# Performance work log

Hardware: AMD Instinct MI355X
Metric: run time of the kernel (lower is better)

Reference implementation:

```python
import jax, jax.numpy as jnp
import numpy as np

K = 512          # fixed candidate budget (replaces dynamic torch.where)
THRESH = 0.6
IOU = 0.5
STRIDE = 2.0
OFFSET = 6.0
WIN = 12.0
SCALE = 0.6      # pyramid scale this pass represents (12/min_face_size)


def _conv(x, w, b):
    y = jax.lax.conv_general_dilated(x, w, (1, 1), 'VALID',
                                     dimension_numbers=('NCHW', 'OIHW', 'NCHW'))
    return y + b[None, :, None, None]


def _prelu(x, a):
    return jnp.where(x >= 0, x, a[None, :, None, None] * x)


def _maxpool2(x):
    return jax.lax.reduce_window(x, -jnp.inf, jax.lax.max,
                                 (1, 1, 2, 2), (1, 1, 2, 2), 'VALID')


def _nms(boxes, valid, thr):
    # torchvision-style greedy NMS over score-sorted boxes; `valid` marks live boxes.
    x1, y1, x2, y2 = boxes[:, 0], boxes[:, 1], boxes[:, 2], boxes[:, 3]
    areas = (x2 - x1) * (y2 - y1)
    n = boxes.shape[0]
    idxs = jnp.arange(n)

    def body(i, keep):
        xi1 = jnp.maximum(x1[i], x1); yi1 = jnp.maximum(y1[i], y1)
        xi2 = jnp.minimum(x2[i], x2); yi2 = jnp.minimum(y2[i], y2)
        inter = jnp.clip(xi2 - xi1, 0.0) * jnp.clip(yi2 - yi1, 0.0)
        iou = inter / (areas[i] + areas - inter + 1e-9)
        sup = (iou > thr) & (idxs > i) & keep[i]
        return keep & (~sup)

    return jax.lax.fori_loop(0, n, body, valid)


def setup_inputs() -> dict:
    key = jax.random.key(0)
    ks = jax.random.split(key, 14)
    d = {}
    d['x'] = jax.random.normal(ks[0], (1, 3, 2048, 2048), dtype=jnp.float32)
    d['w1'] = jax.random.normal(ks[1], (10, 3, 3, 3), dtype=jnp.float32) * 0.1
    d['b1'] = jax.random.normal(ks[2], (10,), dtype=jnp.float32) * 0.01
    d['p1'] = jax.random.uniform(ks[3], (10,), dtype=jnp.float32) * 0.25
    d['w2'] = jax.random.normal(ks[4], (16, 10, 3, 3), dtype=jnp.float32) * 0.1
    d['b2'] = jax.random.normal(ks[5], (16,), dtype=jnp.float32) * 0.01
    d['p2'] = jax.random.uniform(ks[6], (16,), dtype=jnp.float32) * 0.25
    d['w3'] = jax.random.normal(ks[7], (32, 16, 3, 3), dtype=jnp.float32) * 0.1
    d['b3'] = jax.random.normal(ks[8], (32,), dtype=jnp.float32) * 0.01
    d['p3'] = jax.random.uniform(ks[9], (32,), dtype=jnp.float32) * 0.25
    d['wa'] = jax.random.normal(ks[10], (2, 32, 1, 1), dtype=jnp.float32) * 0.1
    d['ba'] = jax.random.normal(ks[11], (2,), dtype=jnp.float32) * 0.01
    d['wb'] = jax.random.normal(ks[12], (4, 32, 1, 1), dtype=jnp.float32) * 0.1
    d['bb'] = jax.random.normal(ks[13], (4,), dtype=jnp.float32) * 0.01
    return d


def reference(x, w1, b1, p1, w2, b2, p2, w3, b3, p3, wa, ba, wb, bb):
    H, W = x.shape[2], x.shape[3]
    h = _prelu(_conv(x, w1, b1), p1)
    h = _maxpool2(h)
    h = _prelu(_conv(h, w2, b2), p2)
    h = _prelu(_conv(h, w3, b3), p3)
    cls = _conv(h, wa, ba)              # [1,2,hf,wf]
    reg = _conv(h, wb, bb)              # [1,4,hf,wf]
    prob = jax.nn.softmax(cls, axis=1)[0, 1]   # Softmax2d over channels, face prob
    hf, wf = prob.shape
    scores = prob.reshape(-1)
    regf = jnp.transpose(reg[0], (1, 2, 0)).reshape(-1, 4)
    # threshold gather -> fixed-size top-K with invalid slots at score -1
    masked = jnp.where(scores >= THRESH, scores, -1.0)
    top_s, idx = jax.lax.top_k(masked, K)
    reg_k = regf[idx]
    yy = (idx // wf).astype(jnp.float32)
    xx = (idx % wf).astype(jnp.float32)
    off_x = ((W - OFFSET * 2) % STRIDE) / 2.0 + OFFSET
    off_y = ((H - OFFSET * 2) % STRIDE) / 2.0 + OFFSET
    cx = (xx * STRIDE + off_x) / SCALE
    cy = (yy * STRIDE + off_y) / SCALE
    ww = WIN / SCALE                    # square 12x12 window / scale
    x1 = cx - ww / 2 + reg_k[:, 0] * ww
    y1 = cy - ww / 2 + reg_k[:, 1] * ww
    x2 = cx + ww / 2 + reg_k[:, 2] * ww
    y2 = cy + ww / 2 + reg_k[:, 3] * ww
    boxes = jnp.stack([x1, y1, x2, y2], axis=1)   # [K,4]
    valid = top_s >= THRESH
    keep = _nms(boxes, valid, IOU)                # per-scale NMS
    keep = _nms(boxes, keep, IOU + 0.2)           # final cross-scale NMS
    out = jnp.concatenate([boxes, top_s[:, None]], axis=1)
    return out * keep[:, None].astype(out.dtype)  # [K,5] boxes+score, zeroed if dropped
```

## Files before the change

### kernel.cpp

```cpp
#include <hip/hip_runtime.h>

typedef unsigned long long u64;
typedef unsigned int u32;

#define W1H 1023
#define W2H 1021
#define W3H 1019
#define NPIX (W3H * W3H)
#define IDXMASK 0xFFFFFull
#define PSTR 1024

#define NBINS 2048
#define HLO 0.3055f
#define HW_ 0.025f
#define HINV 40.0f
#define HDELTA 0.10f

#define W1OFF 0
#define B1OFF 270
#define P1OFF 280
#define W2OFF 290
#define B2OFF 1730
#define P2OFF 1746
#define W3OFF 1762
#define B3OFF 6370
#define P3OFF 6402
#define WAOFF 6434
#define BAOFF 6498
#define WBOFF 6500
#define BBOFF 6628
#define WDTOT 6632

__global__ __launch_bounds__(256) void k_prep(
    const float* __restrict__ w1, const float* __restrict__ b1, const float* __restrict__ p1,
    const float* __restrict__ w2, const float* __restrict__ b2, const float* __restrict__ p2,
    const float* __restrict__ w3, const float* __restrict__ b3, const float* __restrict__ p3,
    const float* __restrict__ wa, const float* __restrict__ ba,
    const float* __restrict__ wb, const float* __restrict__ bb,
    double* __restrict__ wd, int* __restrict__ ctrl, u32* __restrict__ ghist)
{
    int t = threadIdx.x;
    if (t < 2) ctrl[t] = 0;
    for (int i = t; i < NBINS; i += 256) ghist[i] = 0u;
    for (int i = t; i < 270; i += 256)  wd[W1OFF + i] = (double)w1[i];
    if (t < 10) { wd[B1OFF + t] = (double)b1[t]; wd[P1OFF + t] = (double)p1[t]; }
    for (int i = t; i < 1440; i += 256) wd[W2OFF + i] = (double)w2[i];
    if (t < 16) { wd[B2OFF + t] = (double)b2[t]; wd[P2OFF + t] = (double)p2[t]; }
    for (int i = t; i < 4608; i += 256) wd[W3OFF + i] = (double)w3[i];
    if (t < 32) { wd[B3OFF + t] = (double)b3[t]; wd[P3OFF + t] = (double)p3[t]; }
    if (t < 64)  wd[WAOFF + t] = (double)wa[t];
    if (t < 2)   wd[BAOFF + t] = (double)ba[t];
    if (t < 128) wd[WBOFF + t] = (double)wb[t];
    if (t < 4)   wd[BBOFF + t] = (double)bb[t];
}

__global__ __launch_bounds__(256) void k_conv1f(
    const float* __restrict__ x, const float* __restrict__ w1,
    const float* __restrict__ b1, const float* __restrict__ p1,
    float* __restrict__ P)
{
    __shared__ float sw[270];
    __shared__ float sb[10], sp[10];
    int t = threadIdx.y * 64 + threadIdx.x;
    for (int i = t; i < 270; i += 256) sw[i] = w1[i];
    if (t < 10) { sb[t] = b1[t]; sp[t] = p1[t]; }
    __syncthreads();
    int px = blockIdx.x * 64 + threadIdx.x;
    int py = blockIdx.y * 4 + threadIdx.y;
    if (px >= W1H || py >= W1H) return;
    int ix = px * 2, iy = py * 2;
    float acc[10][4];
    #pragma unroll
    for (int ch = 0; ch < 10; ++ch) { acc[ch][0]=0.f; acc[ch][1]=0.f; acc[ch][2]=0.f; acc[ch][3]=0.f; }
    for (int c = 0; c < 3; ++c) {
        float in[4][4];
        #pragma unroll
        for (int u = 0; u < 4; ++u) {
            const float* row = x + ((size_t)c * 2048 + (iy + u)) * 2048 + ix;
            in[u][0]=row[0]; in[u][1]=row[1]; in[u][2]=row[2]; in[u][3]=row[3];
        }
        #pragma unroll
        for (int ch = 0; ch < 10; ++ch) {
            const float* wp = sw + (ch * 3 + c) * 9;
            #pragma unroll
            for (int u = 0; u < 3; ++u)
                #pragma unroll
                for (int v = 0; v < 3; ++v) {
                    float w = wp[u * 3 + v];
                    acc[ch][0] = fmaf(in[u][v],         w, acc[ch][0]);
                    acc[ch][1] = fmaf(in[u][v + 1],     w, acc[ch][1]);
                    acc[ch][2] = fmaf(in[u + 1][v],     w, acc[ch][2]);
                    acc[ch][3] = fmaf(in[u + 1][v + 1], w, acc[ch][3]);
                }
        }
    }
    #pragma unroll
    for (int ch = 0; ch < 10; ++ch) {
        float m = fmaxf(fmaxf(acc[ch][0], acc[ch][1]), fmaxf(acc[ch][2], acc[ch][3])) + sb[ch];
        float r = m >= 0.f ? m : sp[ch] * m;
        P[((size_t)ch * W1H + py) * PSTR + px] = r;
    }
}

__global__ __launch_bounds__(256) void k_conv2f(
    const float* __restrict__ P, const float* __restrict__ w2,
    const float* __restrict__ b2, const float* __restrict__ p2,
    float* __restrict__ H2)
{
    __shared__ __align__(16) float sw[10 * 16 * 12];
    __shared__ float sb[16], sp[16];
    int tx = threadIdx.x, ty = threadIdx.y;
    int t = ty * 64 + tx;
    for (int i = t; i < 1440; i += 256) {
        int o = i / 90, r = i % 90, c = r / 9, k = r % 9;
        sw[(c * 16 + o) * 12 + k] = w2[i];
    }
    if (t < 16) { sb[t] = b2[t]; sp[t] = p2[t]; }
    __syncthreads();
    int py = blockIdx.y;
    int px_base = blockIdx.x * 512 + tx * 8;
    float acc[4][8];
    #pragma unroll
    for (int j = 0; j < 4; ++j)
        #pragma unroll
        for (int p = 0; p < 8; ++p) acc[j][p] = 0.f;

    for (int c = 0; c < 10; ++c) {
        float f[3][12];
        #pragma unroll
        for (int u = 0; u < 3; ++u) {
            const float* row = P + ((size_t)c * W1H + (py + u)) * PSTR + px_base;
            float4 a = *(const float4*)(row);
            float4 b = *(const float4*)(row + 4);
            float4 d = *(const float4*)(row + 8);
            f[u][0]=a.x; f[u][1]=a.y; f[u][2]=a.z;  f[u][3]=a.w;
            f[u][4]=b.x; f[u][5]=b.y; f[u][6]=b.z;  f[u][7]=b.w;
            f[u][8]=d.x; f[u][9]=d.y; f[u][10]=d.z; f[u][11]=d.w;
        }
        #pragma unroll
        for (int j = 0; j < 4; ++j) {
            int o = ty * 4 + j;
            const float4* wv = (const float4*)(sw + (c * 16 + o) * 12);
            float4 wA = wv[0], wB = wv[1], wC = wv[2];
            float w[9] = {wA.x,wA.y,wA.z,wA.w,wB.x,wB.y,wB.z,wB.w,wC.x};
            #pragma unroll
            for (int u = 0; u < 3; ++u)
                #pragma unroll
                for (int v = 0; v < 3; ++v) {
                    float wt = w[u*3+v];
                    #pragma unroll
                    for (int p = 0; p < 8; ++p)
                        acc[j][p] = fmaf(f[u][p+v], wt, acc[j][p]);
                }
        }
    }
    #pragma unroll
    for (int j = 0; j < 4; ++j) {
        int o = ty * 4 + j;
        float bb_ = sb[o], pp_ = sp[o];
        #pragma unroll
        for (int p = 0; p < 8; ++p) {
            int px = px_base + p;
            if (px < W2H) {
                float v = acc[j][p] + bb_;
                v = v >= 0.f ? v : pp_ * v;
                H2[((size_t)o * W2H + py) * PSTR + px] = v;
            }
        }
    }
}

__global__ __launch_bounds__(512, 2) void k_conv3f(
    const float* __restrict__ H2, const float* __restrict__ w3,
    const float* __restrict__ b3, const float* __restrict__ p3,
    const float* __restrict__ wa, const float* __restrict__ ba,
    float* __restrict__ Lg, u32* __restrict__ ghist)
{
    __shared__ __align__(16) float sw[16 * 32 * 12];
    __shared__ float spart[8][512];
    __shared__ u32 hist[NBINS];
    __shared__ float sb[32], sp[32], swd[32];
    __shared__ float slgb;
    int tx = threadIdx.x, ty = threadIdx.y;
    int t = ty * 64 + tx;
    for (int i = t; i < 4608; i += 512) {
        int o = i / 144, rem = i % 144, c = rem / 9, k = rem % 9;
        sw[(c * 32 + o) * 12 + k] = w3[i];
    }
    if (t < 32) { sb[t] = b3[t]; sp[t] = p3[t]; swd[t] = wa[32 + t] - wa[t]; }
    if (t == 0) slgb = ba[1] - ba[0];
    for (int i = t; i < NBINS; i += 512) hist[i] = 0u;
    __syncthreads();

    int py = blockIdx.y;
    int px_base = blockIdx.x * 512 + tx * 8;
    float acc[4][8];
    #pragma unroll
    for (int j = 0; j < 4; ++j)
        #pragma unroll
        for (int p = 0; p < 8; ++p) acc[j][p] = 0.f;

    for (int c = 0; c < 16; ++c) {
        float f[3][12];
        #pragma unroll
        for (int u = 0; u < 3; ++u) {
            const float* row = H2 + ((size_t)c * W2H + (py + u)) * PSTR + px_base;
            float4 a = *(const float4*)(row);
            float4 b = *(const float4*)(row + 4);
            float4 d = *(const float4*)(row + 8);
            f[u][0]=a.x; f[u][1]=a.y; f[u][2]=a.z;  f[u][3]=a.w;
            f[u][4]=b.x; f[u][5]=b.y; f[u][6]=b.z;  f[u][7]=b.w;
            f[u][8]=d.x; f[u][9]=d.y; f[u][10]=d.z; f[u][11]=d.w;
        }
        #pragma unroll
        for (int j = 0; j < 4; ++j) {
            int o = ty * 4 + j;
            const float4* wv = (const float4*)(sw + (c * 32 + o) * 12);
            float4 wA = wv[0], wB = wv[1], wC = wv[2];
            float w[9] = {wA.x,wA.y,wA.z,wA.w,wB.x,wB.y,wB.z,wB.w,wC.x};
            #pragma unroll
            for (int u = 0; u < 3; ++u)
                #pragma unroll
                for (int v = 0; v < 3; ++v) {
                    float wt = w[u*3+v];
                    #pragma unroll
                    for (int p = 0; p < 8; ++p)
                        acc[j][p] = fmaf(f[u][p+v], wt, acc[j][p]);
                }
        }
    }

    float partv[8];
    #pragma unroll
    for (int p = 0; p < 8; ++p) partv[p] = 0.f;
    #pragma unroll
    for (int j = 0; j < 4; ++j) {
        int o = ty * 4 + j;
        float bb_ = sb[o], pp_ = sp[o], wdd = swd[o];
        #pragma unroll
        for (int p = 0; p < 8; ++p) {
            float v = acc[j][p] + bb_;
            v = v >= 0.f ? v : pp_ * v;
            partv[p] = fmaf(wdd, v, partv[p]);
        }
    }
    #pragma unroll
    for (int p = 0; p < 8; ++p) spart[ty][tx * 8 + p] = partv[p];
    __syncthreads();

    {
        float lg = slgb;
        #pragma unroll
        for (int g = 0; g < 8; ++g) lg += spart[g][t];
        int px = blockIdx.x * 512 + t;
        if (px < W3H) {
            Lg[(size_t)py * W3H + px] = lg;
            if (lg >= HLO) {
                int bin = (int)((lg - HLO) * HINV);
                if (bin > NBINS - 1) bin = NBINS - 1;
                atomicAdd(&hist[bin], 1u);
            }
        }
    }
    __syncthreads();
    for (int i = t; i < NBINS; i += 512) {
        u32 v = hist[i];
        if (v) atomicAdd(&ghist[i], v);
    }
}

__global__ __launch_bounds__(256) void k_scan(
    const u32* __restrict__ ghist, int* __restrict__ ctrl)
{
    __shared__ u32 h[NBINS];
    __shared__ u32 tsum[256];
    __shared__ int best;
    int t = threadIdx.x;
    for (int i = t; i < NBINS; i += 256) h[i] = ghist[i];
    if (t == 0) best = -1;
    __syncthreads();
    u32 s = 0;
    #pragma unroll
    for (int k = 0; k < 8; ++k) s += h[t * 8 + k];
    tsum[t] = s;
    __syncthreads();
    for (int off = 1; off < 256; off <<= 1) {
        u32 add = (t + off < 256) ? tsum[t + off] : 0u;
        __syncthreads();
        tsum[t] += add;
        __syncthreads();
    }
    u32 cum = (t < 255) ? tsum[t + 1] : 0u;
    int cand = -1;
    for (int k = 7; k >= 0; --k) {
        cum += h[t * 8 + k];
        if (cand < 0 && cum >= 512) cand = t * 8 + k;
    }
    if (cand >= 0) atomicMax(&best, cand);
    __syncthreads();
    if (t == 0) {
        float T = (best < 0) ? HLO : (HLO + (float)best * HW_ - HDELTA);
        ((float*)ctrl)[2] = T;
    }
}

__global__ __launch_bounds__(256) void k_select(
    const float* __restrict__ Lg, int* __restrict__ ctrl, u32* __restrict__ selidx)
{
    float T = ((const float*)ctrl)[2];
    int stride = gridDim.x * 256;
    for (int i = blockIdx.x * 256 + threadIdx.x; i < NPIX; i += stride) {
        if (Lg[i] >= T) {
            int slot = atomicAdd(&ctrl[0], 1);
            selidx[slot] = (u32)i;
        }
    }
}

__global__ __launch_bounds__(64) void k_recomp(
    const float* __restrict__ x, const double* __restrict__ wd,
    const u32* __restrict__ selidx, int* __restrict__ ctrl,
    u64* __restrict__ keys, double* __restrict__ boxplane)
{
    __shared__ double xw[3][12][12];
    __shared__ double Pw[10][5][5];
    __shared__ double Hw[16][3][3];
    __shared__ double vch[32];
    int nsel = ctrl[0]; if (nsel > NPIX) nsel = NPIX;
    int t = threadIdx.x;
    for (int s = blockIdx.x; s < nsel; s += gridDim.x) {
        u32 idx = selidx[s];
        int y3 = (int)(idx / W3H), x3 = (int)(idx % W3H);
        int xr = 2 * y3, xc = 2 * x3;
        for (int i = t; i < 432; i += 64) {
            int c = i / 144, r = (i % 144) / 12, cc = i % 12;
            xw[c][r][cc] = (double)x[((size_t)c * 2048 + (xr + r)) * 2048 + (xc + cc)];
        }
        __syncthreads();
        for (int i = t; i < 250; i += 64) {
            int ch = i / 25, py = (i % 25) / 5, px = i % 5;
            int r0 = py * 2, c0 = px * 2;
            double a00=0.0, a01=0.0, a10=0.0, a11=0.0;
            for (int c = 0; c < 3; ++c) {
                const double* wp = wd + W1OFF + (ch * 3 + c) * 9;
                #pragma unroll
                for (int u = 0; u < 3; ++u)
                    #pragma unroll
                    for (int v = 0; v < 3; ++v) {
                        double w = wp[u * 3 + v];
                        a00 = fma(xw[c][r0+u][c0+v],     w, a00);
                        a01 = fma(xw[c][r0+u][c0+v+1],   w, a01);
                        a10 = fma(xw[c][r0+u+1][c0+v],   w, a10);
                        a11 = fma(xw[c][r0+u+1][c0+v+1], w, a11);
                    }
            }
            double m = fmax(fmax(a00, a01), fmax(a10, a11)) + wd[B1OFF + ch];
            Pw[ch][py][px] = m >= 0.0 ? m : wd[P1OFF + ch] * m;
        }
        __syncthreads();
        for (int i = t; i < 144; i += 64) {
            int o = i / 9, hy = (i % 9) / 3, hx = i % 3;
            double acc = 0.0;
            for (int c = 0; c < 10; ++c) {
                const double* wp = wd + W2OFF + (o * 10 + c) * 9;
                #pragma unroll
                for (int k = 0; k < 9; ++k)
                    acc = fma(Pw[c][hy + k / 3][hx + k % 3], wp[k], acc);
            }
            acc += wd[B2OFF + o];
            Hw[o][hy][hx] = acc >= 0.0 ? acc : wd[P2OFF + o] * acc;
        }
        __syncthreads();
        if (t < 32) {
            double acc = 0.0;
            for (int c = 0; c < 16; ++c) {
                const double* wp = wd + W3OFF + (t * 16 + c) * 9;
                #pragma unroll
                for (int k = 0; k < 9; ++k)
                    acc = fma(Hw[c][k / 3][k % 3], wp[k], acc);
            }
            acc += wd[B3OFF + t];
            vch[t] = acc >= 0.0 ? acc : wd[P3OFF + t] * acc;
        }
        __syncthreads();
        if (t == 0) {
            double c0 = wd[BAOFF + 0], c1 = wd[BAOFF + 1];
            for (int o = 0; o < 32; ++o) {
                c0 = fma(wd[WAOFF + o], vch[o], c0);
                c1 = fma(wd[WAOFF + 32 + o], vch[o], c1);
            }
            double mx = fmax(c0, c1);
            double e0 = exp(c0 - mx), e1 = exp(c1 - mx);
            double prob = e1 / (e0 + e1);
            if (prob >= 0.6) {
                double r0 = wd[BBOFF+0], r1 = wd[BBOFF+1], r2 = wd[BBOFF+2], r3 = wd[BBOFF+3];
                for (int o = 0; o < 32; ++o) {
                    double v = vch[o];
                    r0 = fma(wd[WBOFF + o], v, r0);
                    r1 = fma(wd[WBOFF + 32 + o], v, r1);
                    r2 = fma(wd[WBOFF + 64 + o], v, r2);
                    r3 = fma(wd[WBOFF + 96 + o], v, r3);
                }
                double fx = (double)x3, fy = (double)y3;
                double cx = (fx * 2.0 + 6.0) / 0.6;
                double cy = (fy * 2.0 + 6.0) / 0.6;
                double ww = 12.0 / 0.6, hw = ww / 2.0;
                double* bp = boxplane + (size_t)idx * 5;
                bp[0] = cx - hw + r0 * ww;
                bp[1] = cy - hw + r1 * ww;
                bp[2] = cx + hw + r2 * ww;
                bp[3] = cy + hw + r3 * ww;
                bp[4] = prob;
                u64 bits = (u64)__double_as_longlong(prob);
                u64 kh = (bits - 0x3FE0000000000000ull) >> 9;
                int slot = atomicAdd(&ctrl[1], 1);
                keys[slot] = (kh << 20) | ((u64)(~idx) & IDXMASK);
            }
        }
        __syncthreads();
    }
}

__global__ __launch_bounds__(512) void k_sortchunks(
    const u64* __restrict__ cand, const int* __restrict__ ctrl,
    u64* __restrict__ sorted)
{
    __shared__ u64 stop_[512];
    __shared__ u64 schunk[512];
    int tid = threadIdx.x;
    int n = ctrl[1]; if (n > NPIX) n = NPIX;
    long base0 = (long)blockIdx.x * 2048;
    stop_[tid] = 0ull;
    if (base0 < n) {
        for (int s = 0; s < 4; ++s) {
            long base = base0 + (long)s * 512;
            if (base >= n) break;
            schunk[tid] = (base + tid < n) ? cand[base + tid] : 0ull;
            for (int k = 2; k <= 512; k <<= 1)
                for (int j = k >> 1; j > 0; j >>= 1) {
                    __syncthreads();
                    int ixj = tid ^ j;
                    if (ixj > tid) {
                        u64 a = schunk[tid], b = schunk[ixj];
                        bool desc = ((tid & k) == 0);
                        if (desc ? (a < b) : (a > b)) { schunk[tid] = b; schunk[ixj] = a; }
                    }
                }
            __syncthreads();
            u64 m = stop_[tid], v = schunk[511 - tid];
            stop_[tid] = m > v ? m : v;
            for (int j = 256; j > 0; j >>= 1) {
                __syncthreads();
                int ixj = tid ^ j;
                if (ixj > tid) {
                    u64 a = stop_[tid], b = stop_[ixj];
                    if (a < b) { stop_[tid] = b; stop_[ixj] = a; }
                }
            }
            __syncthreads();
        }
    }
    sorted[(size_t)blockIdx.x * 512 + tid] = stop_[tid];
}

__global__ __launch_bounds__(512) void k_merge8(
    const u64* __restrict__ in, u64* __restrict__ out, int nin)
{
    __shared__ u64 s[512];
    int tid = threadIdx.x;
    int base = blockIdx.x * 8;
    s[tid] = (base < nin) ? in[(size_t)base * 512 + tid] : 0ull;
    for (int c = 1; c < 8; ++c) {
        int li = base + c;
        u64 v = (li < nin) ? in[(size_t)li * 512 + (511 - tid)] : 0ull;
        __syncthreads();
        u64 m = s[tid];
        s[tid] = m > v ? m : v;
        for (int j = 256; j > 0; j >>= 1) {
            __syncthreads();
            int ixj = tid ^ j;
            if (ixj > tid) {
                u64 a = s[tid], b = s[ixj];
                if (a < b) { s[tid] = b; s[ixj] = a; }
            }
        }
        __syncthreads();
    }
    out[(size_t)blockIdx.x * 512 + tid] = s[tid];
}

__global__ __launch_bounds__(512) void k_boxmat(
    const u64* __restrict__ lists, const double* __restrict__ boxplane,
    u64* __restrict__ mats, double* __restrict__ bxs, u64* __restrict__ validw)
{
    __shared__ double sx1[512], sy1[512], sx2[512], sy2[512], sar[512];
    int tid = threadIdx.x;
    u64 key = lists[tid];
    bool valid = key != 0ull;
    double x1 = 0.0, y1 = 0.0, x2 = 0.0, y2 = 0.0, score = 0.0;
    if (valid) {
        u32 idx = (u32)(IDXMASK - (key & IDXMASK));
        const double* bp = boxplane + (size_t)idx * 5;
        x1 = bp[0]; y1 = bp[1]; x2 = bp[2]; y2 = bp[3]; score = bp[4];
    }
    double area = (x2 - x1) * (y2 - y1);
    sx1[tid] = x1; sy1[tid] = y1; sx2[tid] = x2; sy2[tid] = y2; sar[tid] = area;
    if (blockIdx.x == 0 && blockIdx.y == 0) {
        bxs[tid] = x1; bxs[512 + tid] = y1; bxs[1024 + tid] = x2;
        bxs[1536 + tid] = y2; bxs[2048 + tid] = score;
        u64 bal = __ballot(valid);
        if ((tid & 63) == 0) validw[tid >> 6] = bal;
    }
    __syncthreads();
    double thr = (blockIdx.y == 0) ? 0.5 : 0.7;
    int wv = tid >> 6;
    int rowbase = blockIdx.x * 64;
    for (int r = 0; r < 64; ++r) {
        int i = rowbase + r;
        double ix1 = fmax(sx1[i], x1);
        double iy1 = fmax(sy1[i], y1);
        double ix2 = fmin(sx2[i], x2);
        double iy2 = fmin(sy2[i], y2);
        double inter = fmax(ix2 - ix1, 0.0) * fmax(iy2 - iy1, 0.0);
        double uni = sar[i] + area - inter + 1e-9;
        bool sup = (uni > 0.0) && (inter > thr * uni) && (tid > i);
        u64 w = __ballot(sup);
        if ((tid & 63) == 0)
            mats[((size_t)blockIdx.y * 512 + i) * 8 + wv] = w;
    }
}

__global__ __launch_bounds__(512) void k_nmsfin(
    const u64* __restrict__ mats, const double* __restrict__ bxs,
    const u64* __restrict__ validw, float* __restrict__ out)
{
    __shared__ u64 keepw[8];
    int tid = threadIdx.x;
    if (tid < 8) keepw[tid] = validw[tid];
    __syncthreads();
    for (int pass = 0; pass < 2; ++pass) {
        if (tid < 64) {
            const u64* mat = mats + (size_t)pass * 512 * 8;
            u64 kw = (tid < 8) ? keepw[tid] : 0ull;
            for (int i = 0; i < 512; ++i) {
                u64 row = mat[i * 8 + (tid & 7)];
                u64 cur = __shfl(kw, i >> 6);
                if ((cur >> (i & 63)) & 1) kw &= ~row;
            }
            if (tid < 8) keepw[tid] = kw;
        }
        __syncthreads();
    }
    double kf = ((keepw[tid >> 6] >> (tid & 63)) & 1) ? 1.0 : 0.0;
    out[tid * 5 + 0] = (float)(bxs[tid] * kf);
    out[tid * 5 + 1] = (float)(bxs[512 + tid] * kf);
    out[tid * 5 + 2] = (float)(bxs[1024 + tid] * kf);
    out[tid * 5 + 3] = (float)(bxs[1536 + tid] * kf);
    out[tid * 5 + 4] = (float)(bxs[2048 + tid] * kf);
}

extern "C" void kernel_launch(void* const* d_in, const int* in_sizes, int n_in,
                              void* d_out, int out_size, void* d_ws, size_t ws_size,
                              hipStream_t stream)
{
    const float* x  = (const float*)d_in[0];
    const float* w1 = (const float*)d_in[1];
    const float* b1 = (const float*)d_in[2];
    const float* p1 = (const float*)d_in[3];
    const float* w2 = (const float*)d_in[4];
    const float* b2 = (const float*)d_in[5];
    const float* p2 = (const float*)d_in[6];
    const float* w3 = (const float*)d_in[7];
    const float* b3 = (const float*)d_in[8];
    const float* p3 = (const float*)d_in[9];
    const float* wa = (const float*)d_in[10];
    const float* ba = (const float*)d_in[11];
    const float* wb = (const float*)d_in[12];
    const float* bb = (const float*)d_in[13];
    float* out = (float*)d_out;

    char* ws = (char*)d_ws;
    float*  Pf    = (float*) (ws);
    float*  H2f   = (float*) (ws + 41902080);
    float*  Lg    = (float*) (ws + 108814336);
    u32*    ghist = (u32*)   (ws + 112967936);
    int*    ctrl  = (int*)   (ws + 112976128);
    u32*    selidx= (u32*)   (ws + 112976384);
    u64*    keys  = (u64*)   (ws + 117129984);
    u64*    sorted= (u64*)   (ws + 125437184);
    u64*    l1out = (u64*)   (ws + 127517952);
    u64*    l2out = (u64*)   (ws + 127780096);
    double* boxpl = (double*)(ws + 127812864);
    double* wd    = (double*)(ws + 169347584);
    u64*    l3out = (u64*)   (ws + 125437184);
    u64*    mats  = (u64*)   (ws + 125441280);
    double* bxs   = (double*)(ws + 125506816);
    u64*    vwords= (u64*)   (ws + 125527296);

    k_prep<<<1, 256, 0, stream>>>(w1, b1, p1, w2, b2, p2, w3, b3, p3, wa, ba, wb, bb, wd, ctrl, ghist);
    k_conv1f<<<dim3(16, 256), dim3(64, 4), 0, stream>>>(x, w1, b1, p1, Pf);
    k_conv2f<<<dim3(2, W2H), dim3(64, 4), 0, stream>>>(Pf, w2, b2, p2, H2f);
    k_conv3f<<<dim3(2, W3H), dim3(64, 8), 0, stream>>>(H2f, w3, b3, p3, wa, ba, Lg, ghist);
    k_scan<<<1, 256, 0, stream>>>(ghist, ctrl);
    k_select<<<1024, 256, 0, stream>>>(Lg, ctrl, selidx);
    k_recomp<<<2048, 64, 0, stream>>>(x, wd, selidx, ctrl, keys, boxpl);
    k_sortchunks<<<508, 512, 0, stream>>>(keys, ctrl, sorted);
    k_merge8<<<64, 512, 0, stream>>>(sorted, l1out, 508);
    k_merge8<<<8, 512, 0, stream>>>(l1out, l2out, 64);
    k_merge8<<<1, 512, 0, stream>>>(l2out, l3out, 8);
    k_boxmat<<<dim3(8, 2), 512, 0, stream>>>(l3out, boxpl, mats, bxs, vwords);
    k_nmsfin<<<1, 512, 0, stream>>>(mats, bxs, vwords, out);
}
```

Baseline: 601.0 us.

## Stage conv1 input in LDS, widen conv2/conv3 channel tiles, fuse scan into select

conv1 now loads its input tile into shared memory once, so neighbouring threads no longer issue overlapping scalar global loads. conv2 and conv3 give each thread 8 output channels instead of 4, and each block covers a full row with half as many blocks, so every loaded input row is reused across more channels. The histogram scan is folded into the select kernel, with every block redoing the scan, which removes one launch. The cost is higher register pressure from the 8x8 accumulators, which may lower occupancy, and fewer blocks for conv2 and conv3.

```diff
diff --git a/kernel.cpp b/kernel.cpp
--- a/kernel.cpp
+++ b/kernel.cpp
@@ -61,14 +61,25 @@
 {
     __shared__ float sw[270];
     __shared__ float sb[10], sp[10];
-    int t = threadIdx.y * 64 + threadIdx.x;
+    __shared__ float xs[3][10][132];
+    int tx = threadIdx.x, ty = threadIdx.y;
+    int t = ty * 64 + tx;
     for (int i = t; i < 270; i += 256) sw[i] = w1[i];
     if (t < 10) { sb[t] = b1[t]; sp[t] = p1[t]; }
-    __syncthreads();
-    int px = blockIdx.x * 64 + threadIdx.x;
-    int py = blockIdx.y * 4 + threadIdx.y;
+    int bx = blockIdx.x, by = blockIdx.y;
+    const float4* x4 = (const float4*)x;
+    for (int i = t; i < 990; i += 256) {
+        int c = i / 330, rem = i % 330, r = rem / 33, k = rem % 33;
+        int row = 8 * by + r; if (row > 2047) row = 2047;
+        int col4 = bx * 32 + k; if (col4 > 511) col4 = 511;
+        float4 v = x4[((size_t)c * 2048 + row) * 512 + col4];
+        xs[c][r][k * 4 + 0] = v.x; xs[c][r][k * 4 + 1] = v.y;
+        xs[c][r][k * 4 + 2] = v.z; xs[c][r][k * 4 + 3] = v.w;
+    }
+    __syncthreads();
+    int px = bx * 64 + tx;
+    int py = by * 4 + ty;
     if (px >= W1H || py >= W1H) return;
-    int ix = px * 2, iy = py * 2;
     float acc[10][4];
     #pragma unroll
     for (int ch = 0; ch < 10; ++ch) { acc[ch][0]=0.f; acc[ch][1]=0.f; acc[ch][2]=0.f; acc[ch][3]=0.f; }
@@ -76,8 +87,10 @@
         float in[4][4];
         #pragma unroll
         for (int u = 0; u < 4; ++u) {
-            const float* row = x + ((size_t)c * 2048 + (iy + u)) * 2048 + ix;
-            in[u][0]=row[0]; in[u][1]=row[1]; in[u][2]=row[2]; in[u][3]=row[3];
+            in[u][0] = xs[c][2*ty+u][2*tx+0];
+            in[u][1] = xs[c][2*ty+u][2*tx+1];
+            in[u][2] = xs[c][2*ty+u][2*tx+2];
+            in[u][3] = xs[c][2*ty+u][2*tx+3];
         }
         #pragma unroll
         for (int ch = 0; ch < 10; ++ch) {
@@ -118,10 +131,11 @@
     if (t < 16) { sb[t] = b2[t]; sp[t] = p2[t]; }
     __syncthreads();
     int py = blockIdx.y;
-    int px_base = blockIdx.x * 512 + tx * 8;
-    float acc[4][8];
-    #pragma unroll
-    for (int j = 0; j < 4; ++j)
+    int och0 = (ty & 1) * 8;
+    int px_base = (ty >> 1) * 512 + tx * 8;
+    float acc[8][8];
+    #pragma unroll
+    for (int j = 0; j < 8; ++j)
         #pragma unroll
         for (int p = 0; p < 8; ++p) acc[j][p] = 0.f;
 
@@ -138,8 +152,8 @@
             f[u][8]=d.x; f[u][9]=d.y; f[u][10]=d.z; f[u][11]=d.w;
         }
         #pragma unroll
-        for (int j = 0; j < 4; ++j) {
-            int o = ty * 4 + j;
+        for (int j = 0; j < 8; ++j) {
+            int o = och0 + j;
             const float4* wv = (const float4*)(sw + (c * 16 + o) * 12);
             float4 wA = wv[0], wB = wv[1], wC = wv[2];
             float w[9] = {wA.x,wA.y,wA.z,wA.w,wB.x,wB.y,wB.z,wB.w,wC.x};
@@ -155,8 +169,8 @@
         }
     }
     #pragma unroll
-    for (int j = 0; j < 4; ++j) {
-        int o = ty * 4 + j;
+    for (int j = 0; j < 8; ++j) {
+        int o = och0 + j;
         float bb_ = sb[o], pp_ = sp[o];
         #pragma unroll
         for (int p = 0; p < 8; ++p) {
@@ -177,7 +191,7 @@
     float* __restrict__ Lg, u32* __restrict__ ghist)
 {
     __shared__ __align__(16) float sw[16 * 32 * 12];
-    __shared__ float spart[8][512];
+    __shared__ float spart[4][1024];
     __shared__ u32 hist[NBINS];
     __shared__ float sb[32], sp[32], swd[32];
     __shared__ float slgb;
@@ -193,10 +207,11 @@
     __syncthreads();
 
     int py = blockIdx.y;
-    int px_base = blockIdx.x * 512 + tx * 8;
-    float acc[4][8];
-    #pragma unroll
-    for (int j = 0; j < 4; ++j)
+    int och0 = (ty & 3) * 8;
+    int px_base = (ty >> 2) * 512 + tx * 8;
+    float acc[8][8];
+    #pragma unroll
+    for (int j = 0; j < 8; ++j)
         #pragma unroll
         for (int p = 0; p < 8; ++p) acc[j][p] = 0.f;
 
@@ -213,8 +228,8 @@
             f[u][8]=d.x; f[u][9]=d.y; f[u][10]=d.z; f[u][11]=d.w;
         }
         #pragma unroll
-        for (int j = 0; j < 4; ++j) {
-            int o = ty * 4 + j;
+        for (int j = 0; j < 8; ++j) {
+            int o = och0 + j;
             const float4* wv = (const float4*)(sw + (c * 32 + o) * 12);
             float4 wA = wv[0], wB = wv[1], wC = wv[2];
             float w[9] = {wA.x,wA.y,wA.z,wA.w,wB.x,wB.y,wB.z,wB.w,wC.x};
@@ -234,8 +249,8 @@
     #pragma unroll
     for (int p = 0; p < 8; ++p) partv[p] = 0.f;
     #pragma unroll
-    for (int j = 0; j < 4; ++j) {
-        int o = ty * 4 + j;
+    for (int j = 0; j < 8; ++j) {
+        int o = och0 + j;
         float bb_ = sb[o], pp_ = sp[o], wdd = swd[o];
         #pragma unroll
         for (int p = 0; p < 8; ++p) {
@@ -245,16 +260,17 @@
         }
     }
     #pragma unroll
-    for (int p = 0; p < 8; ++p) spart[ty][tx * 8 + p] = partv[p];
-    __syncthreads();
-
-    {
+    for (int p = 0; p < 8; ++p) spart[ty & 3][px_base + p] = partv[p];
+    __syncthreads();
+
+    #pragma unroll
+    for (int rep = 0; rep < 2; ++rep) {
+        int pl = t + rep * 512;
         float lg = slgb;
         #pragma unroll
-        for (int g = 0; g < 8; ++g) lg += spart[g][t];
-        int px = blockIdx.x * 512 + t;
-        if (px < W3H) {
-            Lg[(size_t)py * W3H + px] = lg;
+        for (int g = 0; g < 4; ++g) lg += spart[g][pl];
+        if (pl < W3H) {
+            Lg[(size_t)py * W3H + pl] = lg;
             if (lg >= HLO) {
                 int bin = (int)((lg - HLO) * HINV);
                 if (bin > NBINS - 1) bin = NBINS - 1;
@@ -269,12 +285,14 @@
     }
 }
 
-__global__ __launch_bounds__(256) void k_scan(
-    const u32* __restrict__ ghist, int* __restrict__ ctrl)
+__global__ __launch_bounds__(256) void k_select(
+    const float* __restrict__ Lg, const u32* __restrict__ ghist,
+    int* __restrict__ ctrl, u32* __restrict__ selidx)
 {
     __shared__ u32 h[NBINS];
     __shared__ u32 tsum[256];
     __shared__ int best;
+    __shared__ float sT;
     int t = threadIdx.x;
     for (int i = t; i < NBINS; i += 256) h[i] = ghist[i];
     if (t == 0) best = -1;
@@ -298,18 +316,11 @@
     }
     if (cand >= 0) atomicMax(&best, cand);
     __syncthreads();
-    if (t == 0) {
-        float T = (best < 0) ? HLO : (HLO + (float)best * HW_ - HDELTA);
-        ((float*)ctrl)[2] = T;
-    }
-}
-
-__global__ __launch_bounds__(256) void k_select(
-    const float* __restrict__ Lg, int* __restrict__ ctrl, u32* __restrict__ selidx)
-{
-    float T = ((const float*)ctrl)[2];
+    if (t == 0) sT = (best < 0) ? HLO : (HLO + (float)best * HW_ - HDELTA);
+    __syncthreads();
+    float T = sT;
     int stride = gridDim.x * 256;
-    for (int i = blockIdx.x * 256 + threadIdx.x; i < NPIX; i += stride) {
+    for (int i = blockIdx.x * 256 + t; i < NPIX; i += stride) {
         if (Lg[i] >= T) {
             int slot = atomicAdd(&ctrl[0], 1);
             selidx[slot] = (u32)i;
@@ -599,10 +610,9 @@
 
     k_prep<<<1, 256, 0, stream>>>(w1, b1, p1, w2, b2, p2, w3, b3, p3, wa, ba, wb, bb, wd, ctrl, ghist);
     k_conv1f<<<dim3(16, 256), dim3(64, 4), 0, stream>>>(x, w1, b1, p1, Pf);
-    k_conv2f<<<dim3(2, W2H), dim3(64, 4), 0, stream>>>(Pf, w2, b2, p2, H2f);
-    k_conv3f<<<dim3(2, W3H), dim3(64, 8), 0, stream>>>(H2f, w3, b3, p3, wa, ba, Lg, ghist);
-    k_scan<<<1, 256, 0, stream>>>(ghist, ctrl);
-    k_select<<<1024, 256, 0, stream>>>(Lg, ctrl, selidx);
+    k_conv2f<<<dim3(1, W2H), dim3(64, 4), 0, stream>>>(Pf, w2, b2, p2, H2f);
+    k_conv3f<<<dim3(1, W3H), dim3(64, 8), 0, stream>>>(H2f, w3, b3, p3, wa, ba, Lg, ghist);
+    k_select<<<1024, 256, 0, stream>>>(Lg, ghist, ctrl, selidx);
     k_recomp<<<2048, 64, 0, stream>>>(x, wd, selidx, ctrl, keys, boxpl);
     k_sortchunks<<<508, 512, 0, stream>>>(keys, ctrl, sorted);
     k_merge8<<<64, 512, 0, stream>>>(sorted, l1out, 508);
```

After: 590.6 us. No clear change (-1.7%).
